# Performance work log

Measured on AMD Instinct MI355X. Metric: run time of the kernel, lower is better.

## Reference

```python
import jax, jax.numpy as jnp
import numpy as np

B, S, D_IN, D_OUT, H = 4, 2048, 1024, 1024, 16
HD = D_OUT // H


def setup_inputs() -> dict:
    key = jax.random.key(0)
    ks = jax.random.split(key, 6)
    s_in = 1.0 / np.sqrt(D_IN)
    s_out = 1.0 / np.sqrt(D_OUT)
    return {
        "x": jax.random.normal(ks[0], (B, S, D_IN), dtype=jnp.float32),
        "Wq": jax.random.uniform(ks[1], (D_IN, D_OUT), jnp.float32, -s_in, s_in),
        "Wk": jax.random.uniform(ks[2], (D_IN, D_OUT), jnp.float32, -s_in, s_in),
        "Wv": jax.random.uniform(ks[3], (D_IN, D_OUT), jnp.float32, -s_in, s_in),
        "Wo": jax.random.uniform(ks[4], (D_OUT, D_OUT), jnp.float32, -s_out, s_out),
        "bo": jax.random.uniform(ks[5], (D_OUT,), jnp.float32, -s_out, s_out),
    }


def reference(x, Wq, Wk, Wv, Wo, bo):
    b, s, _ = x.shape
    # project and split heads: (b, h, s, hd)
    def heads(w):
        return (x @ w).reshape(b, s, H, HD).transpose(0, 2, 1, 3)
    q, k, v = heads(Wq), heads(Wk), heads(Wv)
    scores = jnp.einsum("bhqd,bhkd->bhqk", q, k) / np.sqrt(HD).astype(np.float32)
    causal = jnp.tril(jnp.ones((s, s), dtype=bool))  # True = keep
    scores = jnp.where(causal, scores, -jnp.inf)
    attn = jax.nn.softmax(scores, axis=-1)
    ctx = jnp.einsum("bhqk,bhkd->bhqd", attn, v)
    ctx = ctx.transpose(0, 2, 1, 3).reshape(b, s, D_OUT)
    return ctx @ Wo.T + bo
```

## Files before the change

### kernel.cpp

```cpp
#include <hip/hip_runtime.h>
#include <hip/hip_bf16.h>

#define BB   4
#define SS   2048
#define DIN  1024
#define DOUT 1024
#define NH   16
#define HDIM 64

typedef __hip_bfloat16 bf16;
typedef __attribute__((ext_vector_type(8))) short short8;
typedef __attribute__((ext_vector_type(4))) float floatx4;

#define AS1(p) ((const __attribute__((address_space(1))) void*)(p))
#define AS3(p) ((__attribute__((address_space(3))) void*)(p))

__global__ void cast_f32_bf16_kernel(const float* __restrict__ src, bf16* __restrict__ dst) {
    size_t i = ((size_t)blockIdx.x * 256 + threadIdx.x) * 8;
    float4 a = *(const float4*)(src + i);
    float4 b = *(const float4*)(src + i + 4);
    bf16 o[8] __attribute__((aligned(16)));
    o[0] = __float2bfloat16(a.x); o[1] = __float2bfloat16(a.y);
    o[2] = __float2bfloat16(a.z); o[3] = __float2bfloat16(a.w);
    o[4] = __float2bfloat16(b.x); o[5] = __float2bfloat16(b.y);
    o[6] = __float2bfloat16(b.z); o[7] = __float2bfloat16(b.w);
    *(short8*)(dst + i) = *(short8*)o;
}

__global__ void prep_wqkv_kernel(const float* __restrict__ Wq, const float* __restrict__ Wk,
                                 const float* __restrict__ Wv, bf16* __restrict__ wt) {
    __shared__ float tile[64][65];
    const int kt = blockIdx.x;
    const int nt = blockIdx.y;
    const int k0 = kt * 64, n0 = nt * 64;
    const float* W = (n0 < 1024) ? Wq : (n0 < 2048 ? Wk : Wv);
    const int col0 = n0 & 1023;
    const int tid = threadIdx.x;
    {
        const int kl = tid >> 2, nc = (tid & 3) * 16;
        const float* src = W + (size_t)(k0 + kl) * 1024 + col0 + nc;
        #pragma unroll
        for (int i = 0; i < 16; i += 4) {
            float4 v = *(const float4*)(src + i);
            tile[kl][nc + i + 0] = v.x; tile[kl][nc + i + 1] = v.y;
            tile[kl][nc + i + 2] = v.z; tile[kl][nc + i + 3] = v.w;
        }
    }
    __syncthreads();
    {
        const int nl = tid >> 2, kc = (tid & 3) * 16;
        bf16 o[16] __attribute__((aligned(16)));
        #pragma unroll
        for (int i = 0; i < 16; ++i) o[i] = __float2bfloat16(tile[kc + i][nl]);
        bf16* dst = wt + (size_t)(n0 + nl) * 1024 + k0 + kc;
        *(short8*)dst       = *(short8*)&o[0];
        *(short8*)(dst + 8) = *(short8*)&o[8];
    }
}

template<int EPI>
__global__ __launch_bounds__(256) void gemm_bt_kernel(
    const bf16* __restrict__ A, const bf16* __restrict__ Bt,
    void* __restrict__ C, const float* __restrict__ bias, int K, int ldc) {
    __shared__ __align__(16) bf16 As[128][32];
    __shared__ __align__(16) bf16 Bs[128][32];
    const int tid  = threadIdx.x;
    const int wave = tid >> 6, lane = tid & 63;
    const int lm   = lane & 15, quad = lane >> 4;
    const int wm   = (wave >> 1) * 64, wn = (wave & 1) * 64;
    const size_t rowA0 = (size_t)blockIdx.x * 128;
    const size_t rowB0 = (size_t)blockIdx.y * 128;
    const int srow = wave * 16 + (lane >> 2);
    const int skc  = (lane & 3) * 8;

    floatx4 acc[4][4] = {};

    for (int k0 = 0; k0 < K; k0 += 32) {
        __syncthreads();
        #pragma unroll
        for (int r = 0; r < 2; ++r) {
            const bf16* gA = A  + (rowA0 + r * 64 + srow) * (size_t)K + k0 + skc;
            __builtin_amdgcn_global_load_lds(AS1(gA), AS3(&As[r * 64 + wave * 16][0]), 16, 0, 0);
            const bf16* gB = Bt + (rowB0 + r * 64 + srow) * (size_t)K + k0 + skc;
            __builtin_amdgcn_global_load_lds(AS1(gB), AS3(&Bs[r * 64 + wave * 16][0]), 16, 0, 0);
        }
        __syncthreads();
        short8 a[4], b[4];
        #pragma unroll
        for (int i = 0; i < 4; ++i) a[i] = *(const short8*)&As[wm + i * 16 + lm][quad * 8];
        #pragma unroll
        for (int j = 0; j < 4; ++j) b[j] = *(const short8*)&Bs[wn + j * 16 + lm][quad * 8];
        #pragma unroll
        for (int i = 0; i < 4; ++i)
            #pragma unroll
            for (int j = 0; j < 4; ++j)
                acc[i][j] = __builtin_amdgcn_mfma_f32_16x16x32_bf16(a[i], b[j], acc[i][j], 0, 0, 0);
    }

    #pragma unroll
    for (int i = 0; i < 4; ++i) {
        size_t row = rowA0 + wm + i * 16 + quad * 4;
        #pragma unroll
        for (int j = 0; j < 4; ++j) {
            size_t col = rowB0 + wn + j * 16 + lm;
            float bv = (EPI == 1) ? bias[col] : 0.0f;
            #pragma unroll
            for (int r = 0; r < 4; ++r) {
                if (EPI == 0)
                    ((bf16*)C)[(row + r) * ldc + col] = __float2bfloat16(acc[i][j][r]);
                else
                    ((float*)C)[(row + r) * ldc + col] = acc[i][j][r] + bv;
            }
        }
    }
}

__global__ void transpose_v_kernel(const bf16* __restrict__ qkv, bf16* __restrict__ vt) {
    __shared__ __align__(16) bf16 tile[64][72];
    const int st = blockIdx.x;
    const int bh = blockIdx.y;
    const int b = bh >> 4, h = bh & 15;
    const int s0 = st * 64;
    const int tid = threadIdx.x;
    {
        const int sl = tid >> 2, hc = (tid & 3) * 16;
        const bf16* src = qkv + ((size_t)(b * SS + s0 + sl)) * 3072 + 2048 + h * 64 + hc;
        *(short8*)&tile[sl][hc]     = *(const short8*)src;
        *(short8*)&tile[sl][hc + 8] = *(const short8*)(src + 8);
    }
    __syncthreads();
    {
        const int hl = tid >> 2, sc = (tid & 3) * 16;
        bf16 o[16] __attribute__((aligned(16)));
        #pragma unroll
        for (int i = 0; i < 16; ++i) o[i] = tile[sc + i][hl];
        bf16* dst = vt + ((size_t)(bh * 64 + hl)) * SS + s0 + sc;
        *(short8*)dst       = *(short8*)&o[0];
        *(short8*)(dst + 8) = *(short8*)&o[8];
    }
}

#define PSTR 68
__global__ __launch_bounds__(256, 3) void flash_attn_kernel(
    const bf16* __restrict__ qkv, const bf16* __restrict__ vt, bf16* __restrict__ ctx) {
    __shared__ __align__(16) bf16 Ks[2][64 * 64];
    __shared__ __align__(16) bf16 Vs[2][64 * 64];
    __shared__ __align__(16) bf16 Pl[4][32 * PSTR + 8];
    const int tid  = threadIdx.x;
    const int wave = tid >> 6, lane = tid & 63;
    const int lm   = lane & 15, quad = lane >> 4;

    const int id  = blockIdx.x;
    const int jl  = (id >> 3) & 7;
    const int bh  = (id & 7) * 8 + jl;
    const int p   = 15 - (id >> 6);
    const int b = bh >> 4, h = bh & 15;

    const int lane8r = lane >> 3;
    const int schunk = (lane & 7) ^ lane8r;

    const bf16* kg = qkv + (size_t)b * SS * 3072 + 1024 + h * 64 + schunk * 8;
    const bf16* vg = vt + (size_t)(b * NH + h) * 64 * SS + schunk * 8;

    bf16* Pw = &Pl[wave][0];

    const int qb = p * 128 + wave * 32;
    const int nkt = 2 * p + 2;

    short8 bq[2][2];
    #pragma unroll
    for (int g = 0; g < 2; ++g) {
        const bf16* qp = qkv + ((size_t)(b * SS + qb + g * 16 + lm)) * 3072 + h * 64 + quad * 8;
        bq[g][0] = *(const short8*)qp;
        bq[g][1] = *(const short8*)(qp + 32);
    }

    floatx4 o[2][4] = {};
    float lsum[2] = {0.f, 0.f};

    #pragma unroll
    for (int c = 0; c < 2; ++c) {
        const int row = c * 32 + wave * 8 + lane8r;
        __builtin_amdgcn_global_load_lds(AS1(kg + (size_t)row * 3072), AS3(&Ks[0][(c * 256 + wave * 64) * 8]), 16, 0, 0);
        __builtin_amdgcn_global_load_lds(AS1(vg + (size_t)row * SS), AS3(&Vs[0][(c * 256 + wave * 64) * 8]), 16, 0, 0);
    }

    #pragma unroll 1
    for (int kt = 0; kt < nkt; ++kt) {
        const int cur = kt & 1;
        __syncthreads();
        if (kt + 1 < nkt) {
            #pragma unroll
            for (int c = 0; c < 2; ++c) {
                const int row = c * 32 + wave * 8 + lane8r;
                __builtin_amdgcn_global_load_lds(AS1(kg + (size_t)((kt + 1) * 64 + row) * 3072),
                                                 AS3(&Ks[cur ^ 1][(c * 256 + wave * 64) * 8]), 16, 0, 0);
                __builtin_amdgcn_global_load_lds(AS1(vg + (size_t)row * SS + (kt + 1) * 64),
                                                 AS3(&Vs[cur ^ 1][(c * 256 + wave * 64) * 8]), 16, 0, 0);
            }
        }

        const int sw = lm & 7;
        const bf16* Ksb = &Ks[cur][0];
        const bf16* Vsb = &Vs[cur][0];
        short8 ka[4][2], va[4][2];
        #pragma unroll
        for (int nt = 0; nt < 4; ++nt) {
            const int r0 = (nt * 16 + lm) * 64;
            ka[nt][0] = *(const short8*)(Ksb + r0 + ((quad ^ sw) * 8));
            ka[nt][1] = *(const short8*)(Ksb + r0 + (((4 + quad) ^ sw) * 8));
            va[nt][0] = *(const short8*)(Vsb + r0 + ((quad ^ sw) * 8));
            va[nt][1] = *(const short8*)(Vsb + r0 + (((4 + quad) ^ sw) * 8));
        }

        #pragma unroll
        for (int g = 0; g < 2; ++g) {
            floatx4 sc[4];
            #pragma unroll
            for (int nt = 0; nt < 4; ++nt) {
                floatx4 z = {};
                z = __builtin_amdgcn_mfma_f32_16x16x32_bf16(ka[nt][0], bq[g][0], z, 0, 0, 0);
                z = __builtin_amdgcn_mfma_f32_16x16x32_bf16(ka[nt][1], bq[g][1], z, 0, 0, 0);
                sc[nt] = z;
            }
            if (kt * 64 + 63 > qb + g * 16) {
                const int qrow = qb + g * 16 + lm;
                #pragma unroll
                for (int nt = 0; nt < 4; ++nt)
                    #pragma unroll
                    for (int r = 0; r < 4; ++r)
                        if (kt * 64 + nt * 16 + quad * 4 + r > qrow) sc[nt][r] = -1e30f;
            }
            #pragma unroll
            for (int nt = 0; nt < 4; ++nt) {
                bf16 pk[4] __attribute__((aligned(8)));
                #pragma unroll
                for (int r = 0; r < 4; ++r) {
                    float pv = __builtin_amdgcn_exp2f(sc[nt][r] * 0.18033688f);
                    lsum[g] += pv;
                    pk[r] = __float2bfloat16(pv);
                }
                *(uint64_t*)&Pw[(g * 16 + lm) * PSTR + nt * 16 + quad * 4] = *(uint64_t*)pk;
            }
        }
        #pragma unroll
        for (int g = 0; g < 2; ++g) {
            const short8 ap0 = *(const short8*)&Pw[(g * 16 + lm) * PSTR + quad * 8];
            const short8 ap1 = *(const short8*)&Pw[(g * 16 + lm) * PSTR + 32 + quad * 8];
            #pragma unroll
            for (int t = 0; t < 4; ++t) {
                o[g][t] = __builtin_amdgcn_mfma_f32_16x16x32_bf16(ap0, va[t][0], o[g][t], 0, 0, 0);
                o[g][t] = __builtin_amdgcn_mfma_f32_16x16x32_bf16(ap1, va[t][1], o[g][t], 0, 0, 0);
            }
        }
    }

    #pragma unroll
    for (int g = 0; g < 2; ++g) {
        float rsum = lsum[g];
        rsum += __shfl_xor(rsum, 16);
        rsum += __shfl_xor(rsum, 32);
        float rl[4];
        #pragma unroll
        for (int r = 0; r < 4; ++r) rl[r] = 1.0f / __shfl(rsum, quad * 4 + r);
        #pragma unroll
        for (int t = 0; t < 4; ++t)
            #pragma unroll
            for (int r = 0; r < 4; ++r) {
                size_t row = (size_t)b * SS + qb + g * 16 + quad * 4 + r;
                ctx[row * 1024 + h * 64 + t * 16 + lm] = __float2bfloat16(o[g][t][r] * rl[r]);
            }
    }
}

extern "C" void kernel_launch(void* const* d_in, const int* in_sizes, int n_in,
                              void* d_out, int out_size, void* d_ws, size_t ws_size,
                              hipStream_t stream) {
    const float* x  = (const float*)d_in[0];
    const float* Wq = (const float*)d_in[1];
    const float* Wk = (const float*)d_in[2];
    const float* Wv = (const float*)d_in[3];
    const float* Wo = (const float*)d_in[4];
    const float* bo = (const float*)d_in[5];

    char* ws = (char*)d_ws;
    bf16* xb  = (bf16*)ws;  ws += (size_t)8192 * 1024 * 2;
    bf16* wt  = (bf16*)ws;  ws += (size_t)3072 * 1024 * 2;
    bf16* wob = (bf16*)ws;  ws += (size_t)1024 * 1024 * 2;
    bf16* qkv = (bf16*)ws;  ws += (size_t)8192 * 3072 * 2;
    bf16* vtb = (bf16*)ws;  ws += (size_t)BB * NH * HDIM * SS * 2;
    bf16* ctx = xb;

    cast_f32_bf16_kernel<<<4096, 256, 0, stream>>>(x, xb);
    prep_wqkv_kernel<<<dim3(16, 48), 256, 0, stream>>>(Wq, Wk, Wv, wt);
    cast_f32_bf16_kernel<<<512, 256, 0, stream>>>(Wo, wob);
    gemm_bt_kernel<0><<<dim3(64, 24), 256, 0, stream>>>(xb, wt, (void*)qkv, nullptr, 1024, 3072);
    transpose_v_kernel<<<dim3(32, 64), 256, 0, stream>>>(qkv, vtb);
    flash_attn_kernel<<<1024, 256, 0, stream>>>(qkv, vtb, ctx);
    gemm_bt_kernel<1><<<dim3(64, 8), 256, 0, stream>>>(ctx, wob, d_out, bo, 1024, 1024);
}
```

Measured before the change: 269.6 us.

## Replace QKV projection GEMM with 256x256-tile 8-wave pipelined kernel

Adds a new GEMM kernel for the QKV projection. It uses 256x256 output tiles, 512 threads, and direct global-to-LDS loads into XOR-swizzled, double-buffered shared memory. The main loop is an unrolled 8-phase schedule that interleaves LDS reads, async global prefetch and MFMA quadrants, separated by barriers and priority boosts, and block IDs are remapped for L2 locality. The goal is to raise MFMA utilisation and data reuse over the older 128-tile kernel, at the cost of 128KB of LDS per block and heavy register pressure.

```diff
diff --git a/kernel.cpp b/kernel.cpp
--- a/kernel.cpp
+++ b/kernel.cpp
@@ -115,6 +115,136 @@
     }
 }
 
+__global__ __launch_bounds__(512, 2) void gemm_bt8_kernel(
+    const bf16* __restrict__ A, const bf16* __restrict__ Bt,
+    bf16* __restrict__ C, int K, int ldc) {
+    __shared__ __align__(16) char lds[131072];
+    char* smA = lds;
+    char* smB = lds + 65536;
+
+    const int tid  = threadIdx.x;
+    const int wave = tid >> 6, lane = tid & 63;
+    const int lm   = lane & 15, quad = lane >> 4;
+    const int wm   = wave >> 2, wn = wave & 3;
+
+    const int id  = blockIdx.x;
+    const int q8  = gridDim.x >> 3;
+    const int swz = (id & 7) * q8 + (id >> 3);
+    const size_t rowA0 = (size_t)(swz & 31) * 256;
+    const size_t rowB0 = (size_t)(swz >> 5) * 256;
+
+    const int schunk = (lane & 7) ^ (lane >> 3);
+    const bf16* pAg = A  + (rowA0 + wave * 8 + (lane >> 3)) * (size_t)K + schunk * 8;
+    const bf16* pBg = Bt + (rowB0 + wave * 8 + (lane >> 3)) * (size_t)K + schunk * 8;
+
+    const int ch0 = ((quad)     ^ (lm & 7)) * 16;
+    const int ch1 = ((quad + 4) ^ (lm & 7)) * 16;
+    char* rdA = smA + wm * 16384 + lm * 128;
+    char* rdB = smB + (wn >> 1) * 16384 + (wn & 1) * 8192 + lm * 128;
+
+    short8 aX[4][2], aY[4][2], bn0[2][2][2], bn1[2][2];
+    floatx4 acc[8][4] = {};
+
+#define STGA(buf, half, toff) do { \
+    __builtin_amdgcn_global_load_lds(AS1(pAg + (size_t)((half) * 128 +  0) * K + (toff) * 64), \
+        AS3(smA + (buf) * 32768 + (half) * 16384 +    0 + wave * 1024), 16, 0, 0); \
+    __builtin_amdgcn_global_load_lds(AS1(pAg + (size_t)((half) * 128 + 64) * K + (toff) * 64), \
+        AS3(smA + (buf) * 32768 + (half) * 16384 + 8192 + wave * 1024), 16, 0, 0); \
+} while (0)
+#define STGB(buf, half, toff) do { \
+    __builtin_amdgcn_global_load_lds(AS1(pBg + (size_t)((half) * 128 +  0) * K + (toff) * 64), \
+        AS3(smB + (buf) * 32768 + (half) * 16384 +    0 + wave * 1024), 16, 0, 0); \
+    __builtin_amdgcn_global_load_lds(AS1(pBg + (size_t)((half) * 128 + 64) * K + (toff) * 64), \
+        AS3(smB + (buf) * 32768 + (half) * 16384 + 8192 + wave * 1024), 16, 0, 0); \
+} while (0)
+#define RDA(buf, mq, d) do { \
+    _Pragma("unroll") \
+    for (int f_ = 0; f_ < 4; ++f_) { \
+        d[f_][0] = *(const short8*)(rdA + (buf) * 32768 + (mq) * 8192 + f_ * 2048 + ch0); \
+        d[f_][1] = *(const short8*)(rdA + (buf) * 32768 + (mq) * 8192 + f_ * 2048 + ch1); \
+    } \
+} while (0)
+#define RDB(buf, nq, d) do { \
+    _Pragma("unroll") \
+    for (int n_ = 0; n_ < 2; ++n_) { \
+        d[n_][0] = *(const short8*)(rdB + (buf) * 32768 + (nq) * 4096 + n_ * 2048 + ch0); \
+        d[n_][1] = *(const short8*)(rdB + (buf) * 32768 + (nq) * 4096 + n_ * 2048 + ch1); \
+    } \
+} while (0)
+#define MMQ(a, b, mq, nq) do { \
+    _Pragma("unroll") \
+    for (int f_ = 0; f_ < 4; ++f_) \
+        _Pragma("unroll") \
+        for (int n_ = 0; n_ < 2; ++n_) { \
+            acc[(mq)*4+f_][(nq)*2+n_] = __builtin_amdgcn_mfma_f32_16x16x32_bf16( \
+                a[f_][0], b[n_][0], acc[(mq)*4+f_][(nq)*2+n_], 0, 0, 0); \
+            acc[(mq)*4+f_][(nq)*2+n_] = __builtin_amdgcn_mfma_f32_16x16x32_bf16( \
+                a[f_][1], b[n_][1], acc[(mq)*4+f_][(nq)*2+n_], 0, 0, 0); \
+        } \
+} while (0)
+#define SB0 __builtin_amdgcn_sched_barrier(0)
+#define PHASE(RD, ST, MM) do { \
+    RD; ST; \
+    SB0; __builtin_amdgcn_s_barrier(); SB0; \
+    __builtin_amdgcn_s_setprio(1); MM; __builtin_amdgcn_s_setprio(0); SB0; \
+    asm volatile("s_waitcnt lgkmcnt(0)" ::: "memory"); \
+    asm volatile("s_waitcnt vmcnt(2)" ::: "memory"); \
+    SB0; __builtin_amdgcn_s_barrier(); SB0; \
+} while (0)
+
+    STGA(0, 0, 0); STGA(0, 1, 0); STGB(0, 0, 0); STGB(0, 1, 0);
+    STGA(1, 0, 1); STGA(1, 1, 1); STGB(1, 0, 1);
+    asm volatile("s_waitcnt vmcnt(0)" ::: "memory");
+    SB0; __builtin_amdgcn_s_barrier(); SB0;
+    RDA(0, 0, aX); RDB(0, 0, bn0[0]);
+
+    #pragma unroll 1
+    for (int i = 0; i < (K / 128) - 1; ++i) {
+        PHASE( RDB(0, 1, bn1),    STGB(1, 1, 1), MMQ(aX, bn0[0], 0, 0) );
+        PHASE( RDA(0, 1, aY),     STGB(0, 0, 2), MMQ(aX, bn1,    0, 1) );
+        PHASE( RDA(1, 0, aX),     STGB(0, 1, 2), MMQ(aY, bn1,    1, 1) );
+        PHASE( RDB(1, 0, bn0[1]), STGA(0, 0, 2), MMQ(aY, bn0[0], 1, 0) );
+        PHASE( RDB(1, 1, bn1),    STGA(0, 1, 2), MMQ(aX, bn0[1], 0, 0) );
+        PHASE( RDA(1, 1, aY),     STGB(1, 0, 3), MMQ(aX, bn1,    0, 1) );
+        PHASE( RDA(0, 0, aX),     STGA(1, 0, 3), MMQ(aY, bn1,    1, 1) );
+        PHASE( RDB(0, 0, bn0[0]), STGA(1, 1, 3), MMQ(aY, bn0[1], 1, 0) );
+        pAg += 128; pBg += 128;
+    }
+
+    RDB(0, 1, bn1); STGB(1, 1, 1);
+    SB0; __builtin_amdgcn_s_barrier(); SB0;
+    __builtin_amdgcn_s_setprio(1); MMQ(aX, bn0[0], 0, 0); __builtin_amdgcn_s_setprio(0); SB0;
+    asm volatile("s_waitcnt lgkmcnt(0)" ::: "memory");
+    asm volatile("s_waitcnt vmcnt(0)" ::: "memory");
+    SB0; __builtin_amdgcn_s_barrier(); SB0;
+    RDA(0, 1, aY);      MMQ(aX, bn1,    0, 1);
+    RDA(1, 0, aX);      MMQ(aY, bn1,    1, 1);
+    RDB(1, 0, bn0[1]);  MMQ(aY, bn0[0], 1, 0);
+    RDB(1, 1, bn1);     MMQ(aX, bn0[1], 0, 0);
+    RDA(1, 1, aY);      MMQ(aX, bn1,    0, 1);
+    MMQ(aY, bn1,    1, 1);
+    MMQ(aY, bn0[1], 1, 0);
+
+    #pragma unroll
+    for (int mf = 0; mf < 8; ++mf) {
+        size_t row = rowA0 + wm * 128 + mf * 16 + quad * 4;
+        #pragma unroll
+        for (int nf = 0; nf < 4; ++nf) {
+            size_t col = rowB0 + wn * 64 + nf * 16 + lm;
+            #pragma unroll
+            for (int r = 0; r < 4; ++r)
+                C[(row + r) * ldc + col] = __float2bfloat16(acc[mf][nf][r]);
+        }
+    }
+#undef STGA
+#undef STGB
+#undef RDA
+#undef RDB
+#undef MMQ
+#undef SB0
+#undef PHASE
+}
+
 __global__ void transpose_v_kernel(const bf16* __restrict__ qkv, bf16* __restrict__ vt) {
     __shared__ __align__(16) bf16 tile[64][72];
     const int st = blockIdx.x;
@@ -294,7 +424,7 @@
     cast_f32_bf16_kernel<<<4096, 256, 0, stream>>>(x, xb);
     prep_wqkv_kernel<<<dim3(16, 48), 256, 0, stream>>>(Wq, Wk, Wv, wt);
     cast_f32_bf16_kernel<<<512, 256, 0, stream>>>(Wo, wob);
-    gemm_bt_kernel<0><<<dim3(64, 24), 256, 0, stream>>>(xb, wt, (void*)qkv, nullptr, 1024, 3072);
+    gemm_bt8_kernel<<<384, 512, 0, stream>>>(xb, wt, qkv, 1024, 3072);
     transpose_v_kernel<<<dim3(32, 64), 256, 0, stream>>>(qkv, vtb);
     flash_attn_kernel<<<1024, 256, 0, stream>>>(qkv, vtb, ctx);
     gemm_bt_kernel<1><<<dim3(64, 8), 256, 0, stream>>>(ctx, wob, d_out, bo, 1024, 1024);
```

After: 323.8 us. 20.1% more time.

## Merge prep kernels into one launch and write V transposed from QKV GEMM epilogue

Applied to the files above, without the earlier changes.

Combines the x cast, Wq/Wk/Wv transpose-cast and Wo cast into a single kernel launch that dispatches on block index. Removes the separate V transpose kernel by having the QKV GEMM epilogue write the V columns directly in the transposed per-head layout that attention reads. This drops two launches and one full read/write pass over V. The transposed stores are 8-byte strided writes, which may coalesce less well than the original row stores.

```diff
diff --git a/kernel.cpp b/kernel.cpp
--- a/kernel.cpp
+++ b/kernel.cpp
@@ -15,27 +15,35 @@
 #define AS1(p) ((const __attribute__((address_space(1))) void*)(p))
 #define AS3(p) ((__attribute__((address_space(3))) void*)(p))
 
-__global__ void cast_f32_bf16_kernel(const float* __restrict__ src, bf16* __restrict__ dst) {
-    size_t i = ((size_t)blockIdx.x * 256 + threadIdx.x) * 8;
-    float4 a = *(const float4*)(src + i);
-    float4 b = *(const float4*)(src + i + 4);
-    bf16 o[8] __attribute__((aligned(16)));
-    o[0] = __float2bfloat16(a.x); o[1] = __float2bfloat16(a.y);
-    o[2] = __float2bfloat16(a.z); o[3] = __float2bfloat16(a.w);
-    o[4] = __float2bfloat16(b.x); o[5] = __float2bfloat16(b.y);
-    o[6] = __float2bfloat16(b.z); o[7] = __float2bfloat16(b.w);
-    *(short8*)(dst + i) = *(short8*)o;
-}
-
-__global__ void prep_wqkv_kernel(const float* __restrict__ Wq, const float* __restrict__ Wk,
-                                 const float* __restrict__ Wv, bf16* __restrict__ wt) {
+__global__ void prep_all_kernel(const float* __restrict__ x,
+                                const float* __restrict__ Wq, const float* __restrict__ Wk,
+                                const float* __restrict__ Wv, const float* __restrict__ Wo,
+                                bf16* __restrict__ xb, bf16* __restrict__ wt,
+                                bf16* __restrict__ wob) {
     __shared__ float tile[64][65];
-    const int kt = blockIdx.x;
-    const int nt = blockIdx.y;
+    const int bid = blockIdx.x;
+    const int tid = threadIdx.x;
+    if (bid < 4096 || bid >= 4864) {
+        const float* src = (bid < 4096) ? x : Wo;
+        bf16* dst        = (bid < 4096) ? xb : wob;
+        const int  rb    = (bid < 4096) ? bid : (bid - 4864);
+        size_t i = ((size_t)rb * 256 + tid) * 8;
+        float4 a = *(const float4*)(src + i);
+        float4 b = *(const float4*)(src + i + 4);
+        bf16 o[8] __attribute__((aligned(16)));
+        o[0] = __float2bfloat16(a.x); o[1] = __float2bfloat16(a.y);
+        o[2] = __float2bfloat16(a.z); o[3] = __float2bfloat16(a.w);
+        o[4] = __float2bfloat16(b.x); o[5] = __float2bfloat16(b.y);
+        o[6] = __float2bfloat16(b.z); o[7] = __float2bfloat16(b.w);
+        *(short8*)(dst + i) = *(short8*)o;
+        return;
+    }
+    const int pb = bid - 4096;
+    const int kt = pb & 15;
+    const int nt = pb >> 4;
     const int k0 = kt * 64, n0 = nt * 64;
     const float* W = (n0 < 1024) ? Wq : (n0 < 2048 ? Wk : Wv);
     const int col0 = n0 & 1023;
-    const int tid = threadIdx.x;
     {
         const int kl = tid >> 2, nc = (tid & 3) * 16;
         const float* src = W + (size_t)(k0 + kl) * 1024 + col0 + nc;
@@ -61,7 +69,8 @@
 template<int EPI>
 __global__ __launch_bounds__(256) void gemm_bt_kernel(
     const bf16* __restrict__ A, const bf16* __restrict__ Bt,
-    void* __restrict__ C, const float* __restrict__ bias, int K, int ldc) {
+    void* __restrict__ C, const float* __restrict__ bias, int K, int ldc,
+    bf16* __restrict__ vt) {
     __shared__ __align__(16) bf16 As[128][32];
     __shared__ __align__(16) bf16 Bs[128][32];
     const int tid  = threadIdx.x;
@@ -97,6 +106,25 @@
                 acc[i][j] = __builtin_amdgcn_mfma_f32_16x16x32_bf16(a[i], b[j], acc[i][j], 0, 0, 0);
     }
 
+    if (EPI == 0 && rowB0 >= 2048) {
+        #pragma unroll
+        for (int i = 0; i < 4; ++i) {
+            size_t row = rowA0 + wm + i * 16 + quad * 4;
+            const size_t b = row >> 11;
+            const int    s = (int)(row & 2047);
+            #pragma unroll
+            for (int j = 0; j < 4; ++j) {
+                const int col = (int)(rowB0 - 2048) + wn + j * 16 + lm;
+                bf16 o[4] __attribute__((aligned(8)));
+                #pragma unroll
+                for (int r = 0; r < 4; ++r) o[r] = __float2bfloat16(acc[i][j][r]);
+                *(uint64_t*)(vt + ((b * 16 + (col >> 6)) * 64 + (col & 63)) * (size_t)SS + s)
+                    = *(uint64_t*)o;
+            }
+        }
+        return;
+    }
+
     #pragma unroll
     for (int i = 0; i < 4; ++i) {
         size_t row = rowA0 + wm + i * 16 + quad * 4;
@@ -112,31 +140,6 @@
                     ((float*)C)[(row + r) * ldc + col] = acc[i][j][r] + bv;
             }
         }
-    }
-}
-
-__global__ void transpose_v_kernel(const bf16* __restrict__ qkv, bf16* __restrict__ vt) {
-    __shared__ __align__(16) bf16 tile[64][72];
-    const int st = blockIdx.x;
-    const int bh = blockIdx.y;
-    const int b = bh >> 4, h = bh & 15;
-    const int s0 = st * 64;
-    const int tid = threadIdx.x;
-    {
-        const int sl = tid >> 2, hc = (tid & 3) * 16;
-        const bf16* src = qkv + ((size_t)(b * SS + s0 + sl)) * 3072 + 2048 + h * 64 + hc;
-        *(short8*)&tile[sl][hc]     = *(const short8*)src;
-        *(short8*)&tile[sl][hc + 8] = *(const short8*)(src + 8);
-    }
-    __syncthreads();
-    {
-        const int hl = tid >> 2, sc = (tid & 3) * 16;
-        bf16 o[16] __attribute__((aligned(16)));
-        #pragma unroll
-        for (int i = 0; i < 16; ++i) o[i] = tile[sc + i][hl];
-        bf16* dst = vt + ((size_t)(bh * 64 + hl)) * SS + s0 + sc;
-        *(short8*)dst       = *(short8*)&o[0];
-        *(short8*)(dst + 8) = *(short8*)&o[8];
     }
 }
 
@@ -291,11 +294,8 @@
     bf16* vtb = (bf16*)ws;  ws += (size_t)BB * NH * HDIM * SS * 2;
     bf16* ctx = xb;
 
-    cast_f32_bf16_kernel<<<4096, 256, 0, stream>>>(x, xb);
-    prep_wqkv_kernel<<<dim3(16, 48), 256, 0, stream>>>(Wq, Wk, Wv, wt);
-    cast_f32_bf16_kernel<<<512, 256, 0, stream>>>(Wo, wob);
-    gemm_bt_kernel<0><<<dim3(64, 24), 256, 0, stream>>>(xb, wt, (void*)qkv, nullptr, 1024, 3072);
-    transpose_v_kernel<<<dim3(32, 64), 256, 0, stream>>>(qkv, vtb);
+    prep_all_kernel<<<5376, 256, 0, stream>>>(x, Wq, Wk, Wv, Wo, xb, wt, wob);
+    gemm_bt_kernel<0><<<dim3(64, 24), 256, 0, stream>>>(xb, wt, (void*)qkv, nullptr, 1024, 3072, vtb);
     flash_attn_kernel<<<1024, 256, 0, stream>>>(qkv, vtb, ctx);
-    gemm_bt_kernel<1><<<dim3(64, 8), 256, 0, stream>>>(ctx, wob, d_out, bo, 1024, 1024);
+    gemm_bt_kernel<1><<<dim3(64, 8), 256, 0, stream>>>(ctx, wob, d_out, bo, 1024, 1024, nullptr);
 }
```

After: 262.6 us. -2.6%, faster.
